# Kernel tuning notes

Measured on AMD Instinct MI355X. Metric: run time of the kernel, lower is better.

## Reference

```python
import jax, jax.numpy as jnp
import numpy as np

N = 200000      # nodes
E = 6400000     # edges (avg degree 32)
F_IN = 4        # node feature dim used by GraphConv
H = 184         # 4 * scale(46)
MD_H = 16       # min_distance MLP width
L1 = 188        # H + 4
A = 5           # action_space


def _uniform(k, shape, fan_in):
    b = 1.0 / np.sqrt(fan_in)
    return jax.random.uniform(k, shape, jnp.float32, -b, b)


def setup_inputs() -> dict:
    key = jax.random.key(0)
    ks = jax.random.split(key, 16)
    node_feat = jax.random.normal(ks[0], (N, 6), jnp.float32)
    edge_index = jax.random.randint(ks[1], (2, E), 0, N, dtype=jnp.int32)
    edge_weight = jax.random.uniform(ks[2], (E,), jnp.float32)
    center_idx = 0
    return {
        "node_feat": node_feat,
        "edge_index": edge_index,
        "edge_weight": edge_weight,
        "center_idx": center_idx,
        # GraphConv(4, 184): lin_rel (with bias) applied to aggregated msgs, lin_root (no bias) to x
        "W_rel": _uniform(ks[3], (F_IN, H), F_IN),
        "b_rel": _uniform(ks[4], (H,), F_IN),
        "W_root": _uniform(ks[5], (F_IN, H), F_IN),
        # linear2: 2 -> 16
        "W2": _uniform(ks[6], (2, MD_H), 2),
        "b2": _uniform(ks[7], (MD_H,), 2),
        # linear2_1: 16 -> 16
        "W21": _uniform(ks[8], (MD_H, MD_H), MD_H),
        "b21": _uniform(ks[9], (MD_H,), MD_H),
        # linear1: 200 -> 188
        "W1": _uniform(ks[10], (H + MD_H, L1), H + MD_H),
        "b1": _uniform(ks[11], (L1,), H + MD_H),
        # linear4: 188 -> 5
        "W4": _uniform(ks[12], (L1, A), L1),
        "b4": _uniform(ks[13], (A,), L1),
    }


def reference(node_feat, edge_index, edge_weight, center_idx,
              W_rel, b_rel, W_root, W2, b2, W21, b21, W1, b1, W4, b4):
    x = node_feat[:, :4]                                   # [N, 4]
    src, dst = edge_index[0], edge_index[1]
    # GraphConv message: e_ji * x_j, mean-aggregated at target nodes
    msg = x[src] * edge_weight[:, None]                    # [E, 4]
    agg = jax.ops.segment_sum(msg, dst, num_segments=N)    # [N, 4]
    deg = jax.ops.segment_sum(jnp.ones((E,), jnp.float32), dst, num_segments=N)
    mean = agg / jnp.maximum(deg, 1.0)[:, None]
    h = jax.nn.relu(mean @ W_rel + b_rel + x @ W_root)     # [N, 184]
    # global_max_pool with batch=None -> max over all nodes
    x1 = jnp.max(h, axis=0, keepdims=True)                 # [1, 184]
    x2 = h[center_idx:center_idx + 1]                      # [1, 184]
    g = x2 - x1
    md = node_feat[center_idx, 4:].reshape(1, 2)           # [1, 2]
    md = jax.nn.relu(md @ W2 + b2)
    md = jax.nn.relu(md @ W21 + b21)
    g = jnp.concatenate([g, md], axis=1)                   # [1, 200]
    g = jax.nn.relu(g @ W1 + b1)
    return g @ W4 + b4                                     # [1, 5]
```

## Files before the change

kernel.cpp:

```cpp
#include <hip/hip_runtime.h>

#define H 184
#define MDH 16
#define L1D 188
#define BBITS 9
#define BSZ 512
#define KMAX 512
#define CHUNKE 4096
#define SSUB 4
#define SREC_CAP 4416
#define HREC 2240
#define HRPT 5
#define NSPLIT 4

__global__ void zero_kernel(int* __restrict__ p, int n) {
    int i = blockIdx.x * blockDim.x + threadIdx.x;
    if (i < n) p[i] = 0;
}

__global__ __launch_bounds__(256) void pack_kernel(
        const float* __restrict__ nf, float4* __restrict__ x4,
        int* __restrict__ zp, int zn, int N) {
    __shared__ float s[256 * 6];
    int base = blockIdx.x * 256;
    int t = threadIdx.x;
    if (blockIdx.x == 0 && zp != nullptr)
        for (int i = t; i < zn; i += 256) zp[i] = 0;
    for (int i = t; i < 256 * 6; i += 256) {
        int gi = base * 6 + i;
        s[i] = (gi < N * 6) ? nf[gi] : 0.0f;
    }
    __syncthreads();
    int n = base + t;
    if (n < N)
        x4[n] = make_float4(s[t * 6], s[t * 6 + 1], s[t * 6 + 2], s[t * 6 + 3]);
}

__device__ __forceinline__ void scan512_w8(const int* __restrict__ cnt,
                                           int* __restrict__ sc,
                                           int* __restrict__ wtot, int t) {
    int wv = t >> 6, ln = t & 63;
    int x = cnt[t];
    #pragma unroll
    for (int d = 1; d < 64; d <<= 1) {
        int y = __shfl_up(x, d, 64);
        if (ln >= d) x += y;
    }
    if (ln == 63) wtot[wv] = x;
    __syncthreads();
    int woff = 0;
    #pragma unroll
    for (int wq = 0; wq < 7; ++wq) woff += (wq < wv) ? wtot[wq] : 0;
    sc[t] = woff + x;
    __syncthreads();
}

__global__ __launch_bounds__(512, 8) void partition_cs_kernel(
        const int* __restrict__ ei, const float* __restrict__ ew,
        int* __restrict__ cursor, uint2* __restrict__ region,
        const float* __restrict__ nf, float4* __restrict__ x4,
        int E, int K, int CAP, int N, int npack) {
    __shared__ uint2 srec[CHUNKE];
    __shared__ int cnt[KMAX];
    __shared__ int sc[KMAX];
    __shared__ int wbase[KMAX];
    __shared__ int wtot[8];
    int t = threadIdx.x;
    int c = blockIdx.x;

    if (c < npack) {
        float* sp = (float*)srec;
        int base = c * 256;
        for (int i = t; i < 256 * 6; i += 512) {
            int gi = base * 6 + i;
            sp[i] = (gi < N * 6) ? nf[gi] : 0.0f;
        }
        __syncthreads();
        if (t < 256) {
            int n = base + t;
            if (n < N)
                x4[n] = make_float4(sp[t * 6], sp[t * 6 + 1],
                                    sp[t * 6 + 2], sp[t * 6 + 3]);
        }
    }

    int e0 = c * CHUNKE;
    int e1 = min(E, e0 + CHUNKE);

    cnt[t] = 0;
    __syncthreads();

    unsigned meta[8];
    unsigned srcv[8];
    unsigned wv[8];
    #pragma unroll
    for (int j = 0; j < 2; ++j) {
        int e = e0 + t * 4 + j * 2048;
        int4 d4 = make_int4(0, 0, 0, 0);
        int4 s4 = make_int4(0, 0, 0, 0);
        float4 w4 = make_float4(0.f, 0.f, 0.f, 0.f);
        bool full = (e + 3 < e1);
        if (full) {
            d4 = *(const int4*)(ei + E + e);
            s4 = *(const int4*)(ei + e);
            w4 = *(const float4*)(ew + e);
        }
        #pragma unroll
        for (int q = 0; q < 4; ++q) {
            int idx = j * 4 + q;
            meta[idx] = 0xFFFFFFFFu;
            int eq = e + q;
            if (eq < e1) {
                int dst = full ? (q == 0 ? d4.x : q == 1 ? d4.y : q == 2 ? d4.z : d4.w)
                               : ei[E + eq];
                int src = full ? (q == 0 ? s4.x : q == 1 ? s4.y : q == 2 ? s4.z : s4.w)
                               : ei[eq];
                float w = full ? (q == 0 ? w4.x : q == 1 ? w4.y : q == 2 ? w4.z : w4.w)
                               : ew[eq];
                int k = ((unsigned)dst) >> BBITS;
                int r = atomicAdd(&cnt[k], 1);
                meta[idx] = ((unsigned)k << 21) | ((unsigned)r << 9)
                          | ((unsigned)dst & (BSZ - 1));
                srcv[idx] = (unsigned)src;
                wv[idx]   = __float_as_uint(w);
            }
        }
    }
    __syncthreads();

    scan512_w8(cnt, sc, wtot, t);

    {
        int ck = cnt[t];
        int pos = sc[t] - ck;
        int b = 0;
        if (t < K && ck > 0) {
            b = atomicAdd(&cursor[t], ck);
            if (b + ck > CAP) b = CAP - ck;
        }
        wbase[t] = b;
        cnt[t] = pos;
    }
    __syncthreads();

    #pragma unroll
    for (int j = 0; j < 8; ++j) {
        if (meta[j] != 0xFFFFFFFFu) {
            int k  = meta[j] >> 21;
            int r  = (meta[j] >> 9) & 0xFFF;
            int dl = meta[j] & (BSZ - 1);
            int slot = cnt[k] + r;
            srec[slot] = make_uint2(((unsigned)dl << 18) | srcv[j], wv[j]);
        }
    }
    __syncthreads();

    {
        int pos = cnt[t];
        int ck = sc[t] - pos;
        if (t < K && ck > 0) {
            uint2* dstp = region + (size_t)t * CAP + wbase[t];
            for (int i = 0; i < ck; ++i)
                dstp[i] = srec[pos + i];
        }
    }
}

__global__ __launch_bounds__(512, 8) void bucket_sort_accum_kernel(
        const float4* __restrict__ x4, const uint2* __restrict__ region,
        const int* __restrict__ cursor, float* __restrict__ partials, int CAP) {
    __shared__ float4 sxw[HREC];
    __shared__ int cnt[BSZ], sc[BSZ];
    __shared__ int wtot[8];
    int k = blockIdx.x / SSUB;
    int s = blockIdx.x % SSUB;
    int t = threadIdx.x;

    int len = cursor[k];
    if (len > CAP) len = CAP;
    const uint2* base = region + (size_t)k * CAP;
    int i0 = (int)(((long long)len * s) / SSUB);
    int i1 = (int)(((long long)len * (s + 1)) / SSUB);
    int span = i1 - i0;

    float4 acc = make_float4(0.f, 0.f, 0.f, 0.f);
    int degc = 0;

    #pragma unroll
    for (int half = 0; half < 2; ++half) {
        int h0 = i0 + (span * half) / 2;
        int h1 = i0 + (span * (half + 1)) / 2;
        cnt[t] = 0;
        __syncthreads();

        float4 xw[HRPT];
        unsigned rb[HRPT];
        #pragma unroll
        for (int j = 0; j < HRPT; ++j) {
            int i = h0 + t + j * 512;
            rb[j] = 0xFFFFFFFFu;
            if (i < h1) {
                uint2 r = base[i];
                int bin = r.x >> 18;
                float4 xv = x4[r.x & 0x3FFFFu];
                float w = __uint_as_float(r.y);
                xw[j] = make_float4(xv.x * w, xv.y * w, xv.z * w, xv.w * w);
                int rk = atomicAdd(&cnt[bin], 1);
                rb[j] = ((unsigned)bin << 13) | (unsigned)rk;
            }
        }
        __syncthreads();

        scan512_w8(cnt, sc, wtot, t);

        #pragma unroll
        for (int j = 0; j < HRPT; ++j) {
            if (rb[j] != 0xFFFFFFFFu) {
                int bin = rb[j] >> 13;
                int rk  = rb[j] & 0x1FFF;
                sxw[sc[bin] - cnt[bin] + rk] = xw[j];
            }
        }
        __syncthreads();

        int c = cnt[t], st = sc[t] - c;
        for (int i = 0; i < c; ++i) {
            float4 v = sxw[st + i];
            acc.x += v.x; acc.y += v.y; acc.z += v.z; acc.w += v.w;
        }
        degc += c;
        __syncthreads();
    }

    float* pp = partials + (size_t)blockIdx.x * (BSZ * 5);
    pp[0 * BSZ + t] = acc.x;
    pp[1 * BSZ + t] = acc.y;
    pp[2 * BSZ + t] = acc.z;
    pp[3 * BSZ + t] = acc.w;
    pp[4 * BSZ + t] = (float)degc;
}

__global__ __launch_bounds__(256) void edge_atomic_kernel(
        const float* __restrict__ nf, const int* __restrict__ ei,
        const float* __restrict__ ew, float* __restrict__ agg,
        float* __restrict__ deg, int E) {
    int e = blockIdx.x * blockDim.x + threadIdx.x;
    if (e >= E) return;
    int src = ei[e];
    int dst = ei[E + e];
    float w = ew[e];
    const float2* xr = (const float2*)(nf + (size_t)src * 6);
    float2 x01 = xr[0];
    float2 x23 = xr[1];
    float* a = agg + (size_t)dst * 4;
    atomicAdd(a + 0, x01.x * w);
    atomicAdd(a + 1, x01.y * w);
    atomicAdd(a + 2, x23.x * w);
    atomicAdd(a + 3, x23.y * w);
    atomicAdd(deg + dst, 1.0f);
}

__global__ __launch_bounds__(256) void node_bucket_kernel(
        const float4* __restrict__ x4,
        const float* __restrict__ partials,
        const float* __restrict__ W_rel, const float* __restrict__ b_rel,
        const float* __restrict__ W_root,
        const int*   __restrict__ centerp,
        unsigned int* __restrict__ xmax_bits,
        float* __restrict__ h0,
        int N) {
    __shared__ float4 xm[BSZ / NSPLIT];
    __shared__ float4 xt[BSZ / NSPLIT];
    const int NB = BSZ / NSPLIT;
    int k = blockIdx.x / NSPLIT;
    int q = blockIdx.x % NSPLIT;
    int t = threadIdx.x;
    int center = *centerp;
    int base_d = q * NB;
    int nmax = min(BSZ, N - (k << BBITS));
    int cnt_local = min(NB, nmax - base_d);
    if (cnt_local <= 0) return;
    const float* bp = partials + (size_t)k * SSUB * (BSZ * 5);

    if (t < NB) {
        int d = base_d + t;
        float a0 = 0.f, a1 = 0.f, a2 = 0.f, a3 = 0.f, dg = 0.f;
        #pragma unroll
        for (int s = 0; s < SSUB; ++s) {
            const float* p = bp + (size_t)s * (BSZ * 5);
            a0 += p[0 * BSZ + d];
            a1 += p[1 * BSZ + d];
            a2 += p[2 * BSZ + d];
            a3 += p[3 * BSZ + d];
            dg += p[4 * BSZ + d];
        }
        float inv = 1.0f / fmaxf(dg, 1.0f);
        xm[t] = make_float4(a0 * inv, a1 * inv, a2 * inv, a3 * inv);
    } else {
        int i = t - NB;
        int n = (k << BBITS) + base_d + i;
        xt[i] = (n < N) ? x4[n] : make_float4(0.f, 0.f, 0.f, 0.f);
    }
    __syncthreads();

    int j = t;
    if (j >= H) return;

    float wr0 = W_rel[0 * H + j], wr1 = W_rel[1 * H + j];
    float wr2 = W_rel[2 * H + j], wr3 = W_rel[3 * H + j];
    float wo0 = W_root[0 * H + j], wo1 = W_root[1 * H + j];
    float wo2 = W_root[2 * H + j], wo3 = W_root[3 * H + j];
    float b = b_rel[j];

    int cd = ((center >> BBITS) == k) ? (center & (BSZ - 1)) - base_d : -1;
    float mx = 0.0f;
    for (int i = 0; i < cnt_local; ++i) {
        float4 m = xm[i];
        float4 x = xt[i];
        float v = b
                + m.x * wr0 + m.y * wr1 + m.z * wr2 + m.w * wr3
                + x.x * wo0 + x.y * wo1 + x.z * wo2 + x.w * wo3;
        v = fmaxf(v, 0.0f);
        mx = fmaxf(mx, v);
        if (i == cd) h0[j] = v;
    }
    atomicMax(xmax_bits + j, __float_as_uint(mx));
}

__global__ __launch_bounds__(192) void node_kernel(
        const float4* __restrict__ x4,
        const float* __restrict__ agg,
        const float* __restrict__ deg,
        const float* __restrict__ W_rel, const float* __restrict__ b_rel,
        const float* __restrict__ W_root,
        const int*   __restrict__ centerp,
        unsigned int* __restrict__ xmax_bits,
        float* __restrict__ h0,
        int N, int nodes_per_block) {
    int j = threadIdx.x;
    if (j >= H) return;
    int center = *centerp;
    int n0 = blockIdx.x * nodes_per_block;
    int n1 = n0 + nodes_per_block;
    if (n1 > N) n1 = N;

    float wr0 = W_rel[0 * H + j], wr1 = W_rel[1 * H + j];
    float wr2 = W_rel[2 * H + j], wr3 = W_rel[3 * H + j];
    float wo0 = W_root[0 * H + j], wo1 = W_root[1 * H + j];
    float wo2 = W_root[2 * H + j], wo3 = W_root[3 * H + j];
    float b = b_rel[j];

    float mx = 0.0f;
    for (int n = n0; n < n1; ++n) {
        float4 a = ((const float4*)agg)[n];
        float inv = 1.0f / fmaxf(deg[n], 1.0f);
        float4 x = x4[n];
        float v = b
                + (a.x * inv) * wr0 + (a.y * inv) * wr1
                + (a.z * inv) * wr2 + (a.w * inv) * wr3
                + x.x * wo0 + x.y * wo1 + x.z * wo2 + x.w * wo3;
        v = fmaxf(v, 0.0f);
        mx = fmaxf(mx, v);
        if (n == center) h0[j] = v;
    }
    atomicMax(xmax_bits + j, __float_as_uint(mx));
}

__global__ __launch_bounds__(768) void final_kernel(
        const float* __restrict__ nf,
        const int*   __restrict__ centerp,
        const unsigned int* __restrict__ xmax_bits,
        const float* __restrict__ h0,
        const float* __restrict__ W2,  const float* __restrict__ b2,
        const float* __restrict__ W21, const float* __restrict__ b21,
        const float* __restrict__ W1,  const float* __restrict__ b1,
        const float* __restrict__ W4,  const float* __restrict__ b4,
        float* __restrict__ out) {
    __shared__ float gin[H + MDH];
    __shared__ float md0[MDH];
    __shared__ float part[4][L1D];
    __shared__ float g1[L1D];
    int t = threadIdx.x;
    int center = *centerp;

    if (t < H) gin[t] = h0[t] - __uint_as_float(xmax_bits[t]);
    if (t < MDH) {
        float m0 = nf[(size_t)center * 6 + 4];
        float m1 = nf[(size_t)center * 6 + 5];
        md0[t] = fmaxf(m0 * W2[t] + m1 * W2[MDH + t] + b2[t], 0.0f);
    }
    __syncthreads();
    if (t < MDH) {
        float s = b21[t];
        for (int k = 0; k < MDH; ++k) s += md0[k] * W21[k * MDH + t];
        gin[H + t] = fmaxf(s, 0.0f);
    }
    __syncthreads();

    {
        int kc = t / 192;
        int j  = t - kc * 192;
        if (j < L1D) {
            float s = 0.0f;
            int k0 = kc * 50, k1 = k0 + 50;
            #pragma unroll 5
            for (int k = k0; k < k1; ++k) s += gin[k] * W1[k * L1D + j];
            part[kc][j] = s;
        }
    }
    __syncthreads();
    if (t < L1D)
        g1[t] = fmaxf(part[0][t] + part[1][t] + part[2][t] + part[3][t] + b1[t],
                      0.0f);
    __syncthreads();

    int w = t >> 6, ln = t & 63;
    if (w < 5) {
        float s = 0.0f;
        for (int k = ln; k < L1D; k += 64) s += g1[k] * W4[k * 5 + w];
        #pragma unroll
        for (int d = 32; d > 0; d >>= 1) s += __shfl_down(s, d, 64);
        if (ln == 0) out[w] = s + b4[w];
    }
}

extern "C" void kernel_launch(void* const* d_in, const int* in_sizes, int n_in,
                              void* d_out, int out_size, void* d_ws, size_t ws_size,
                              hipStream_t stream) {
    const float* nf      = (const float*)d_in[0];
    const int*   ei      = (const int*)  d_in[1];
    const float* ew      = (const float*)d_in[2];
    const int*   centerp = (const int*)  d_in[3];
    const float* W_rel   = (const float*)d_in[4];
    const float* b_rel   = (const float*)d_in[5];
    const float* W_root  = (const float*)d_in[6];
    const float* W2      = (const float*)d_in[7];
    const float* b2      = (const float*)d_in[8];
    const float* W21     = (const float*)d_in[9];
    const float* b21     = (const float*)d_in[10];
    const float* W1      = (const float*)d_in[11];
    const float* b1      = (const float*)d_in[12];
    const float* W4      = (const float*)d_in[13];
    const float* b4      = (const float*)d_in[14];
    float* out = (float*)d_out;

    const int N = in_sizes[0] / 6;
    const int E = in_sizes[1] / 2;
    const int K = (N + BSZ - 1) >> BBITS;
    const int nchunks = (E + CHUNKE - 1) / CHUNKE;
    const int npack = (N + 255) / 256;
    int cap = E / K + E / K / 16 + 256;
    cap = (cap + 63) & ~63;

    int*          cursor   = (int*)d_ws;
    unsigned int* xmax     = (unsigned int*)(cursor + 512);
    float*        h0       = (float*)(xmax + H);
    float*        agg      = h0 + H;
    float*        deg      = agg + (size_t)N * 4;
    float4*       x4       = (float4*)(deg + N);
    float*        partials = (float*)(x4 + N);
    uint2*        region   = (uint2*)(partials + (size_t)K * SSUB * (BSZ * 5));

    size_t need = (size_t)((char*)(region + (size_t)K * cap) - (char*)d_ws);
    bool fast = (ws_size >= need) && (K <= KMAX) && (N <= (1 << 18))
             && ((E & 3) == 0)
             && ((cap + SSUB - 1) / SSUB <= SREC_CAP)
             && (((cap + SSUB - 1) / SSUB + 1) / 2 <= HREC)
             && (npack <= nchunks);

    if (fast) {
        hipMemsetAsync(cursor, 0, (size_t)(512 + H) * sizeof(int), stream);
        partition_cs_kernel<<<nchunks, 512, 0, stream>>>(ei, ew, cursor, region,
                                                         nf, x4, E, K, cap,
                                                         N, npack);
        bucket_sort_accum_kernel<<<K * SSUB, 512, 0, stream>>>(x4, region, cursor,
                                                               partials, cap);
        node_bucket_kernel<<<K * NSPLIT, 256, 0, stream>>>(x4, partials,
                                                           W_rel, b_rel, W_root,
                                                           centerp, xmax, h0, N);
    } else {
        const int blocks = 2048;
        const int npb = (N + blocks - 1) / blocks;
        zero_kernel<<<(N * 5 + 255) / 256, 256, 0, stream>>>((int*)agg, N * 5);
        zero_kernel<<<1, 256, 0, stream>>>(cursor, 512 + H);
        pack_kernel<<<(N + 255) / 256, 256, 0, stream>>>(nf, x4, nullptr, 0, N);
        edge_atomic_kernel<<<(E + 255) / 256, 256, 0, stream>>>(nf, ei, ew, agg, deg, E);
        node_kernel<<<blocks, 192, 0, stream>>>(x4, agg, deg,
                                                W_rel, b_rel, W_root,
                                                centerp, xmax, h0, N, npb);
    }

    final_kernel<<<1, 768, 0, stream>>>(nf, centerp, xmax, h0,
                                        W2, b2, W21, b21, W1, b1, W4, b4, out);
}
```

Before: 270.1 us.

## Defer src/weight loads to scatter phase and split partition launch in two

The partition kernel now loads only destination indices before the histogram and scan, and reads source indices and weights later, just before writing the shared-memory records. This cuts the per-thread register arrays held across the barriers, which may raise occupancy, but it puts the src and weight loads after the synchronisations, where they are harder to overlap. The partition grid is also split into two launches with a block offset, which adds launch overhead and a serialisation point between the halves.

```diff
diff --git a/kernel.cpp b/kernel.cpp
--- a/kernel.cpp
+++ b/kernel.cpp
@@ -59,14 +59,14 @@
         const int* __restrict__ ei, const float* __restrict__ ew,
         int* __restrict__ cursor, uint2* __restrict__ region,
         const float* __restrict__ nf, float4* __restrict__ x4,
-        int E, int K, int CAP, int N, int npack) {
+        int E, int K, int CAP, int N, int npack, int c0) {
     __shared__ uint2 srec[CHUNKE];
     __shared__ int cnt[KMAX];
     __shared__ int sc[KMAX];
     __shared__ int wbase[KMAX];
     __shared__ int wtot[8];
     int t = threadIdx.x;
-    int c = blockIdx.x;
+    int c = blockIdx.x + c0;
 
     if (c < npack) {
         float* sp = (float*)srec;
@@ -91,20 +91,12 @@
     __syncthreads();
 
     unsigned meta[8];
-    unsigned srcv[8];
-    unsigned wv[8];
     #pragma unroll
     for (int j = 0; j < 2; ++j) {
         int e = e0 + t * 4 + j * 2048;
         int4 d4 = make_int4(0, 0, 0, 0);
-        int4 s4 = make_int4(0, 0, 0, 0);
-        float4 w4 = make_float4(0.f, 0.f, 0.f, 0.f);
         bool full = (e + 3 < e1);
-        if (full) {
-            d4 = *(const int4*)(ei + E + e);
-            s4 = *(const int4*)(ei + e);
-            w4 = *(const float4*)(ew + e);
-        }
+        if (full) d4 = *(const int4*)(ei + E + e);
         #pragma unroll
         for (int q = 0; q < 4; ++q) {
             int idx = j * 4 + q;
@@ -113,16 +105,10 @@
             if (eq < e1) {
                 int dst = full ? (q == 0 ? d4.x : q == 1 ? d4.y : q == 2 ? d4.z : d4.w)
                                : ei[E + eq];
-                int src = full ? (q == 0 ? s4.x : q == 1 ? s4.y : q == 2 ? s4.z : s4.w)
-                               : ei[eq];
-                float w = full ? (q == 0 ? w4.x : q == 1 ? w4.y : q == 2 ? w4.z : w4.w)
-                               : ew[eq];
                 int k = ((unsigned)dst) >> BBITS;
                 int r = atomicAdd(&cnt[k], 1);
                 meta[idx] = ((unsigned)k << 21) | ((unsigned)r << 9)
                           | ((unsigned)dst & (BSZ - 1));
-                srcv[idx] = (unsigned)src;
-                wv[idx]   = __float_as_uint(w);
             }
         }
     }
@@ -144,13 +130,30 @@
     __syncthreads();
 
     #pragma unroll
-    for (int j = 0; j < 8; ++j) {
-        if (meta[j] != 0xFFFFFFFFu) {
-            int k  = meta[j] >> 21;
-            int r  = (meta[j] >> 9) & 0xFFF;
-            int dl = meta[j] & (BSZ - 1);
-            int slot = cnt[k] + r;
-            srec[slot] = make_uint2(((unsigned)dl << 18) | srcv[j], wv[j]);
+    for (int j = 0; j < 2; ++j) {
+        int e = e0 + t * 4 + j * 2048;
+        int4 s4 = make_int4(0, 0, 0, 0);
+        float4 w4 = make_float4(0.f, 0.f, 0.f, 0.f);
+        bool full = (e + 3 < e1);
+        if (full) {
+            s4 = *(const int4*)(ei + e);
+            w4 = *(const float4*)(ew + e);
+        }
+        #pragma unroll
+        for (int q = 0; q < 4; ++q) {
+            int idx = j * 4 + q;
+            int eq = e + q;
+            if (meta[idx] != 0xFFFFFFFFu) {
+                int src = full ? (q == 0 ? s4.x : q == 1 ? s4.y : q == 2 ? s4.z : s4.w)
+                               : ei[eq];
+                float w = full ? (q == 0 ? w4.x : q == 1 ? w4.y : q == 2 ? w4.z : w4.w)
+                               : ew[eq];
+                int k  = meta[idx] >> 21;
+                int r  = (meta[idx] >> 9) & 0xFFF;
+                int dl = meta[idx] & (BSZ - 1);
+                srec[cnt[k] + r] = make_uint2(((unsigned)dl << 18) | (unsigned)src,
+                                              __float_as_uint(w));
+            }
         }
     }
     __syncthreads();
@@ -462,17 +465,22 @@
     uint2*        region   = (uint2*)(partials + (size_t)K * SSUB * (BSZ * 5));
 
     size_t need = (size_t)((char*)(region + (size_t)K * cap) - (char*)d_ws);
+    const int nb1 = (nchunks + 1) / 2;
+    const int nb2 = nchunks - nb1;
     bool fast = (ws_size >= need) && (K <= KMAX) && (N <= (1 << 18))
              && ((E & 3) == 0)
              && ((cap + SSUB - 1) / SSUB <= SREC_CAP)
              && (((cap + SSUB - 1) / SSUB + 1) / 2 <= HREC)
-             && (npack <= nchunks);
+             && (npack <= nb1) && (nb2 > 0);
 
     if (fast) {
         hipMemsetAsync(cursor, 0, (size_t)(512 + H) * sizeof(int), stream);
-        partition_cs_kernel<<<nchunks, 512, 0, stream>>>(ei, ew, cursor, region,
-                                                         nf, x4, E, K, cap,
-                                                         N, npack);
+        partition_cs_kernel<<<nb1, 512, 0, stream>>>(ei, ew, cursor, region,
+                                                     nf, x4, E, K, cap,
+                                                     N, npack, 0);
+        partition_cs_kernel<<<nb2, 512, 0, stream>>>(ei, ew, cursor, region,
+                                                     nf, x4, E, K, cap,
+                                                     N, npack, nb1);
         bucket_sort_accum_kernel<<<K * SSUB, 512, 0, stream>>>(x4, region, cursor,
                                                                partials, cap);
         node_bucket_kernel<<<K * NSPLIT, 256, 0, stream>>>(x4, partials,
```

After: 292.7 us. 8.4% more time.

## Fuse bucket accumulation with node transform into a single per-bucket kernel

Applied to the files above, without the earlier changes.

Merges the bucketed edge accumulation and the per-node GraphConv, ReLU and max kernel into one kernel with one block per destination bucket. Each block now walks its whole bucket in shared-memory-sized chunks instead of splitting it across four sub-blocks. This removes the partials buffer round-trip through global memory and one kernel launch. The cost is four times fewer blocks during the gather-heavy accumulation phase, so there is less parallelism to hide memory latency. Capacity guards tied to the old split are dropped.

```diff
diff --git a/kernel.cpp b/kernel.cpp
--- a/kernel.cpp
+++ b/kernel.cpp
@@ -8,10 +8,8 @@
 #define KMAX 512
 #define CHUNKE 4096
 #define SSUB 4
-#define SREC_CAP 4416
 #define HREC 2240
 #define HRPT 5
-#define NSPLIT 4
 
 __global__ void zero_kernel(int* __restrict__ p, int n) {
     int i = blockIdx.x * blockDim.x + threadIdx.x;
@@ -149,8 +147,7 @@
             int k  = meta[j] >> 21;
             int r  = (meta[j] >> 9) & 0xFFF;
             int dl = meta[j] & (BSZ - 1);
-            int slot = cnt[k] + r;
-            srec[slot] = make_uint2(((unsigned)dl << 18) | srcv[j], wv[j]);
+            srec[cnt[k] + r] = make_uint2(((unsigned)dl << 18) | srcv[j], wv[j]);
         }
     }
     __syncthreads();
@@ -166,30 +163,30 @@
     }
 }
 
-__global__ __launch_bounds__(512, 8) void bucket_sort_accum_kernel(
+__global__ __launch_bounds__(512, 8) void accum_node_kernel(
         const float4* __restrict__ x4, const uint2* __restrict__ region,
-        const int* __restrict__ cursor, float* __restrict__ partials, int CAP) {
+        const int* __restrict__ cursor,
+        const float* __restrict__ W_rel, const float* __restrict__ b_rel,
+        const float* __restrict__ W_root,
+        const int*   __restrict__ centerp,
+        unsigned int* __restrict__ xmax_bits,
+        float* __restrict__ h0,
+        int CAP, int N) {
     __shared__ float4 sxw[HREC];
     __shared__ int cnt[BSZ], sc[BSZ];
     __shared__ int wtot[8];
-    int k = blockIdx.x / SSUB;
-    int s = blockIdx.x % SSUB;
+    int k = blockIdx.x;
     int t = threadIdx.x;
 
     int len = cursor[k];
     if (len > CAP) len = CAP;
     const uint2* base = region + (size_t)k * CAP;
-    int i0 = (int)(((long long)len * s) / SSUB);
-    int i1 = (int)(((long long)len * (s + 1)) / SSUB);
-    int span = i1 - i0;
 
     float4 acc = make_float4(0.f, 0.f, 0.f, 0.f);
     int degc = 0;
 
-    #pragma unroll
-    for (int half = 0; half < 2; ++half) {
-        int h0 = i0 + (span * half) / 2;
-        int h1 = i0 + (span * (half + 1)) / 2;
+    for (int c0 = 0; c0 < len; c0 += HREC) {
+        int c1 = min(len, c0 + HREC);
         cnt[t] = 0;
         __syncthreads();
 
@@ -197,9 +194,9 @@
         unsigned rb[HRPT];
         #pragma unroll
         for (int j = 0; j < HRPT; ++j) {
-            int i = h0 + t + j * 512;
+            int i = c0 + t + j * 512;
             rb[j] = 0xFFFFFFFFu;
-            if (i < h1) {
+            if (i < c1) {
                 uint2 r = base[i];
                 int bin = r.x >> 18;
                 float4 xv = x4[r.x & 0x3FFFFu];
@@ -232,12 +229,44 @@
         __syncthreads();
     }
 
-    float* pp = partials + (size_t)blockIdx.x * (BSZ * 5);
-    pp[0 * BSZ + t] = acc.x;
-    pp[1 * BSZ + t] = acc.y;
-    pp[2 * BSZ + t] = acc.z;
-    pp[3 * BSZ + t] = acc.w;
-    pp[4 * BSZ + t] = (float)degc;
+    float4* xm = sxw;
+    float4* xt = sxw + BSZ;
+    int n = (k << BBITS) + t;
+    float inv = 1.0f / fmaxf((float)degc, 1.0f);
+    xm[t] = make_float4(acc.x * inv, acc.y * inv, acc.z * inv, acc.w * inv);
+    xt[t] = (n < N) ? x4[n] : make_float4(0.f, 0.f, 0.f, 0.f);
+    __syncthreads();
+
+    int nmax = min(BSZ, N - (k << BBITS));
+    int center = *centerp;
+    int cloc = ((center >> BBITS) == k) ? (center & (BSZ - 1)) : -1;
+    float* pm = (float*)cnt;
+    int halfg = (t >= 256) ? 1 : 0;
+    int j = t - halfg * 256;
+    if (j < H) {
+        float wr0 = W_rel[0 * H + j], wr1 = W_rel[1 * H + j];
+        float wr2 = W_rel[2 * H + j], wr3 = W_rel[3 * H + j];
+        float wo0 = W_root[0 * H + j], wo1 = W_root[1 * H + j];
+        float wo2 = W_root[2 * H + j], wo3 = W_root[3 * H + j];
+        float b = b_rel[j];
+        int ibeg = halfg * 256;
+        int iend = min(ibeg + 256, nmax);
+        float mx = 0.0f;
+        for (int i = ibeg; i < iend; ++i) {
+            float4 m = xm[i];
+            float4 x = xt[i];
+            float v = b
+                    + m.x * wr0 + m.y * wr1 + m.z * wr2 + m.w * wr3
+                    + x.x * wo0 + x.y * wo1 + x.z * wo2 + x.w * wo3;
+            v = fmaxf(v, 0.0f);
+            mx = fmaxf(mx, v);
+            if (i == cloc) h0[j] = v;
+        }
+        pm[halfg * H + j] = mx;
+    }
+    __syncthreads();
+    if (t < H)
+        atomicMax(xmax_bits + t, __float_as_uint(fmaxf(pm[t], pm[H + t])));
 }
 
 __global__ __launch_bounds__(256) void edge_atomic_kernel(
@@ -258,73 +287,6 @@
     atomicAdd(a + 2, x23.x * w);
     atomicAdd(a + 3, x23.y * w);
     atomicAdd(deg + dst, 1.0f);
-}
-
-__global__ __launch_bounds__(256) void node_bucket_kernel(
-        const float4* __restrict__ x4,
-        const float* __restrict__ partials,
-        const float* __restrict__ W_rel, const float* __restrict__ b_rel,
-        const float* __restrict__ W_root,
-        const int*   __restrict__ centerp,
-        unsigned int* __restrict__ xmax_bits,
-        float* __restrict__ h0,
-        int N) {
-    __shared__ float4 xm[BSZ / NSPLIT];
-    __shared__ float4 xt[BSZ / NSPLIT];
-    const int NB = BSZ / NSPLIT;
-    int k = blockIdx.x / NSPLIT;
-    int q = blockIdx.x % NSPLIT;
-    int t = threadIdx.x;
-    int center = *centerp;
-    int base_d = q * NB;
-    int nmax = min(BSZ, N - (k << BBITS));
-    int cnt_local = min(NB, nmax - base_d);
-    if (cnt_local <= 0) return;
-    const float* bp = partials + (size_t)k * SSUB * (BSZ * 5);
-
-    if (t < NB) {
-        int d = base_d + t;
-        float a0 = 0.f, a1 = 0.f, a2 = 0.f, a3 = 0.f, dg = 0.f;
-        #pragma unroll
-        for (int s = 0; s < SSUB; ++s) {
-            const float* p = bp + (size_t)s * (BSZ * 5);
-            a0 += p[0 * BSZ + d];
-            a1 += p[1 * BSZ + d];
-            a2 += p[2 * BSZ + d];
-            a3 += p[3 * BSZ + d];
-            dg += p[4 * BSZ + d];
-        }
-        float inv = 1.0f / fmaxf(dg, 1.0f);
-        xm[t] = make_float4(a0 * inv, a1 * inv, a2 * inv, a3 * inv);
-    } else {
-        int i = t - NB;
-        int n = (k << BBITS) + base_d + i;
-        xt[i] = (n < N) ? x4[n] : make_float4(0.f, 0.f, 0.f, 0.f);
-    }
-    __syncthreads();
-
-    int j = t;
-    if (j >= H) return;
-
-    float wr0 = W_rel[0 * H + j], wr1 = W_rel[1 * H + j];
-    float wr2 = W_rel[2 * H + j], wr3 = W_rel[3 * H + j];
-    float wo0 = W_root[0 * H + j], wo1 = W_root[1 * H + j];
-    float wo2 = W_root[2 * H + j], wo3 = W_root[3 * H + j];
-    float b = b_rel[j];
-
-    int cd = ((center >> BBITS) == k) ? (center & (BSZ - 1)) - base_d : -1;
-    float mx = 0.0f;
-    for (int i = 0; i < cnt_local; ++i) {
-        float4 m = xm[i];
-        float4 x = xt[i];
-        float v = b
-                + m.x * wr0 + m.y * wr1 + m.z * wr2 + m.w * wr3
-                + x.x * wo0 + x.y * wo1 + x.z * wo2 + x.w * wo3;
-        v = fmaxf(v, 0.0f);
-        mx = fmaxf(mx, v);
-        if (i == cd) h0[j] = v;
-    }
-    atomicMax(xmax_bits + j, __float_as_uint(mx));
 }
 
 __global__ __launch_bounds__(192) void node_kernel(
@@ -464,8 +426,6 @@
     size_t need = (size_t)((char*)(region + (size_t)K * cap) - (char*)d_ws);
     bool fast = (ws_size >= need) && (K <= KMAX) && (N <= (1 << 18))
              && ((E & 3) == 0)
-             && ((cap + SSUB - 1) / SSUB <= SREC_CAP)
-             && (((cap + SSUB - 1) / SSUB + 1) / 2 <= HREC)
              && (npack <= nchunks);
 
     if (fast) {
@@ -473,11 +433,9 @@
         partition_cs_kernel<<<nchunks, 512, 0, stream>>>(ei, ew, cursor, region,
                                                          nf, x4, E, K, cap,
                                                          N, npack);
-        bucket_sort_accum_kernel<<<K * SSUB, 512, 0, stream>>>(x4, region, cursor,
-                                                               partials, cap);
-        node_bucket_kernel<<<K * NSPLIT, 256, 0, stream>>>(x4, partials,
-                                                           W_rel, b_rel, W_root,
-                                                           centerp, xmax, h0, N);
+        accum_node_kernel<<<K, 512, 0, stream>>>(x4, region, cursor,
+                                                 W_rel, b_rel, W_root,
+                                                 centerp, xmax, h0, cap, N);
     } else {
         const int blocks = 2048;
         const int npb = (N + blocks - 1) / blocks;
```

Result: slower. 276.0 us (+2.2%).

## Fuse bucket accumulation, node transform and final MLP into one cooperative kernel

Applied to the files above, without the earlier changes.

Replaces the bucket_sort_accum, node_bucket and final kernels with a single cooperative-launch kernel that processes the same work items in grid-stride loops, separated by grid-wide syncs. The goal is to remove two kernel launches and the gaps between them. The cost is two grid.sync barriers, a persistent grid of 768–1024 blocks that may be less balanced than the original launch shapes, and dependence on cooperative launch succeeding. If that launch fails, the code falls back to the old three-kernel path.

```diff
diff --git a/kernel.cpp b/kernel.cpp
--- a/kernel.cpp
+++ b/kernel.cpp
@@ -1,4 +1,7 @@
 #include <hip/hip_runtime.h>
+#include <hip/hip_cooperative_groups.h>
+
+namespace cg = cooperative_groups;
 
 #define H 184
 #define MDH 16
@@ -8,7 +11,6 @@
 #define KMAX 512
 #define CHUNKE 4096
 #define SSUB 4
-#define SREC_CAP 4416
 #define HREC 2240
 #define HRPT 5
 #define NSPLIT 4
@@ -149,8 +151,7 @@
             int k  = meta[j] >> 21;
             int r  = (meta[j] >> 9) & 0xFFF;
             int dl = meta[j] & (BSZ - 1);
-            int slot = cnt[k] + r;
-            srec[slot] = make_uint2(((unsigned)dl << 18) | srcv[j], wv[j]);
+            srec[cnt[k] + r] = make_uint2(((unsigned)dl << 18) | srcv[j], wv[j]);
         }
     }
     __syncthreads();
@@ -162,6 +163,201 @@
             uint2* dstp = region + (size_t)t * CAP + wbase[t];
             for (int i = 0; i < ck; ++i)
                 dstp[i] = srec[pos + i];
+        }
+    }
+}
+
+__global__ __launch_bounds__(512, 8) void fused_tail_kernel(
+        const float4* __restrict__ x4, const uint2* __restrict__ region,
+        const int* __restrict__ cursor, float* __restrict__ partials,
+        const float* __restrict__ W_rel, const float* __restrict__ b_rel,
+        const float* __restrict__ W_root,
+        const int*   __restrict__ centerp,
+        unsigned int* __restrict__ xmax_bits, float* __restrict__ h0,
+        const float* __restrict__ nf,
+        const float* __restrict__ W2,  const float* __restrict__ b2,
+        const float* __restrict__ W21, const float* __restrict__ b21,
+        const float* __restrict__ W1,  const float* __restrict__ b1,
+        const float* __restrict__ W4,  const float* __restrict__ b4,
+        float* __restrict__ out,
+        int CAP, int N, int K, int nitems) {
+    __shared__ float4 sxw[HREC];
+    __shared__ int cnt[BSZ], sc[BSZ];
+    __shared__ int wtot[8];
+    cg::grid_group grid = cg::this_grid();
+    int t = threadIdx.x;
+
+    for (int wi = blockIdx.x; wi < nitems; wi += gridDim.x) {
+        int k = wi / SSUB, s = wi - (wi / SSUB) * SSUB;
+        int len = cursor[k];
+        if (len > CAP) len = CAP;
+        const uint2* rbase = region + (size_t)k * CAP;
+        int i0 = (int)(((long long)len * s) / SSUB);
+        int i1 = (int)(((long long)len * (s + 1)) / SSUB);
+        int span = i1 - i0;
+
+        float4 acc = make_float4(0.f, 0.f, 0.f, 0.f);
+        int degc = 0;
+
+        #pragma unroll
+        for (int half = 0; half < 2; ++half) {
+            int hb = i0 + (span * half) / 2;
+            int he = i0 + (span * (half + 1)) / 2;
+            cnt[t] = 0;
+            __syncthreads();
+
+            float4 xw[HRPT];
+            unsigned rb[HRPT];
+            #pragma unroll
+            for (int j = 0; j < HRPT; ++j) {
+                int i = hb + t + j * 512;
+                rb[j] = 0xFFFFFFFFu;
+                if (i < he) {
+                    uint2 r = rbase[i];
+                    int bin = r.x >> 18;
+                    float4 xv = x4[r.x & 0x3FFFFu];
+                    float w = __uint_as_float(r.y);
+                    xw[j] = make_float4(xv.x * w, xv.y * w, xv.z * w, xv.w * w);
+                    int rk = atomicAdd(&cnt[bin], 1);
+                    rb[j] = ((unsigned)bin << 13) | (unsigned)rk;
+                }
+            }
+            __syncthreads();
+
+            scan512_w8(cnt, sc, wtot, t);
+
+            #pragma unroll
+            for (int j = 0; j < HRPT; ++j) {
+                if (rb[j] != 0xFFFFFFFFu) {
+                    int bin = rb[j] >> 13;
+                    int rk  = rb[j] & 0x1FFF;
+                    sxw[sc[bin] - cnt[bin] + rk] = xw[j];
+                }
+            }
+            __syncthreads();
+
+            int c = cnt[t], st = sc[t] - c;
+            for (int i = 0; i < c; ++i) {
+                float4 v = sxw[st + i];
+                acc.x += v.x; acc.y += v.y; acc.z += v.z; acc.w += v.w;
+            }
+            degc += c;
+            __syncthreads();
+        }
+
+        float* pp = partials + (size_t)wi * (BSZ * 5);
+        pp[0 * BSZ + t] = acc.x;
+        pp[1 * BSZ + t] = acc.y;
+        pp[2 * BSZ + t] = acc.z;
+        pp[3 * BSZ + t] = acc.w;
+        pp[4 * BSZ + t] = (float)degc;
+    }
+
+    grid.sync();
+
+    int center = *centerp;
+    for (int wi = blockIdx.x; wi < K * NSPLIT; wi += gridDim.x) {
+        int k = wi >> 2, q = wi & 3;
+        int base_d = q * 128;
+        float4* xm = sxw;
+        float4* xt = sxw + 128;
+        if (t < 128) {
+            int d = base_d + t;
+            float a0 = 0.f, a1 = 0.f, a2 = 0.f, a3 = 0.f, dg = 0.f;
+            const float* bp = partials + (size_t)k * SSUB * (BSZ * 5);
+            #pragma unroll
+            for (int s = 0; s < SSUB; ++s) {
+                const float* p = bp + (size_t)s * (BSZ * 5);
+                a0 += p[0 * BSZ + d];
+                a1 += p[1 * BSZ + d];
+                a2 += p[2 * BSZ + d];
+                a3 += p[3 * BSZ + d];
+                dg += p[4 * BSZ + d];
+            }
+            float inv = 1.0f / fmaxf(dg, 1.0f);
+            xm[t] = make_float4(a0 * inv, a1 * inv, a2 * inv, a3 * inv);
+        } else if (t < 256) {
+            int i = t - 128;
+            int n = (k << BBITS) + base_d + i;
+            xt[i] = (n < N) ? x4[n] : make_float4(0.f, 0.f, 0.f, 0.f);
+        }
+        __syncthreads();
+
+        int nmax = min(BSZ, N - (k << BBITS));
+        int cnt_local = min(128, nmax - base_d);
+        float* pm = (float*)cnt;
+        int halfg = (t >= 256) ? 1 : 0;
+        int j = t - halfg * 256;
+        if (cnt_local > 0 && j < H) {
+            float wr0 = W_rel[0 * H + j], wr1 = W_rel[1 * H + j];
+            float wr2 = W_rel[2 * H + j], wr3 = W_rel[3 * H + j];
+            float wo0 = W_root[0 * H + j], wo1 = W_root[1 * H + j];
+            float wo2 = W_root[2 * H + j], wo3 = W_root[3 * H + j];
+            float b = b_rel[j];
+            int cloc = ((center >> BBITS) == k) ? (center & (BSZ - 1)) - base_d : -1;
+            int ib = halfg * 64;
+            int ie = min(ib + 64, cnt_local);
+            float mx = 0.0f;
+            for (int i = ib; i < ie; ++i) {
+                float4 m = xm[i];
+                float4 x = xt[i];
+                float v = b
+                        + m.x * wr0 + m.y * wr1 + m.z * wr2 + m.w * wr3
+                        + x.x * wo0 + x.y * wo1 + x.z * wo2 + x.w * wo3;
+                v = fmaxf(v, 0.0f);
+                mx = fmaxf(mx, v);
+                if (i == cloc) h0[j] = v;
+            }
+            pm[halfg * H + j] = mx;
+        }
+        __syncthreads();
+        if (cnt_local > 0 && t < H)
+            atomicMax(xmax_bits + t, __float_as_uint(fmaxf(pm[t], pm[H + t])));
+        __syncthreads();
+    }
+
+    grid.sync();
+
+    if (blockIdx.x == 0) {
+        float* gin = (float*)sxw;
+        float* md0 = gin + 256;
+        float* pt  = md0 + 32;
+        float* g1  = pt + 2 * L1D;
+        if (t < H) gin[t] = h0[t] - __uint_as_float(xmax_bits[t]);
+        if (t < MDH) {
+            float m0 = nf[(size_t)center * 6 + 4];
+            float m1 = nf[(size_t)center * 6 + 5];
+            md0[t] = fmaxf(m0 * W2[t] + m1 * W2[MDH + t] + b2[t], 0.0f);
+        }
+        __syncthreads();
+        if (t < MDH) {
+            float s2 = b21[t];
+            for (int kk = 0; kk < MDH; ++kk) s2 += md0[kk] * W21[kk * MDH + t];
+            gin[H + t] = fmaxf(s2, 0.0f);
+        }
+        __syncthreads();
+        {
+            int kc = t >> 8;
+            int j  = t & 255;
+            if (j < L1D) {
+                float s2 = 0.0f;
+                int k0 = kc * 100, k1 = k0 + 100;
+                #pragma unroll 4
+                for (int kk = k0; kk < k1; ++kk) s2 += gin[kk] * W1[kk * L1D + j];
+                pt[kc * L1D + j] = s2;
+            }
+        }
+        __syncthreads();
+        if (t < L1D)
+            g1[t] = fmaxf(pt[t] + pt[L1D + t] + b1[t], 0.0f);
+        __syncthreads();
+        int w = t >> 6, ln = t & 63;
+        if (w < 5) {
+            float s2 = 0.0f;
+            for (int kk = ln; kk < L1D; kk += 64) s2 += g1[kk] * W4[kk * 5 + w];
+            #pragma unroll
+            for (int d = 32; d > 0; d >>= 1) s2 += __shfl_down(s2, d, 64);
+            if (ln == 0) out[w] = s2 + b4[w];
         }
     }
 }
@@ -188,8 +384,8 @@
 
     #pragma unroll
     for (int half = 0; half < 2; ++half) {
-        int h0 = i0 + (span * half) / 2;
-        int h1 = i0 + (span * (half + 1)) / 2;
+        int h0i = i0 + (span * half) / 2;
+        int h1i = i0 + (span * (half + 1)) / 2;
         cnt[t] = 0;
         __syncthreads();
 
@@ -197,9 +393,9 @@
         unsigned rb[HRPT];
         #pragma unroll
         for (int j = 0; j < HRPT; ++j) {
-            int i = h0 + t + j * 512;
+            int i = h0i + t + j * 512;
             rb[j] = 0xFFFFFFFFu;
-            if (i < h1) {
+            if (i < h1i) {
                 uint2 r = base[i];
                 int bin = r.x >> 18;
                 float4 xv = x4[r.x & 0x3FFFFu];
@@ -210,9 +406,7 @@
             }
         }
         __syncthreads();
-
         scan512_w8(cnt, sc, wtot, t);
-
         #pragma unroll
         for (int j = 0; j < HRPT; ++j) {
             if (rb[j] != 0xFFFFFFFFu) {
@@ -222,7 +416,6 @@
             }
         }
         __syncthreads();
-
         int c = cnt[t], st = sc[t] - c;
         for (int i = 0; i < c; ++i) {
             float4 v = sxw[st + i];
@@ -238,26 +431,6 @@
     pp[2 * BSZ + t] = acc.z;
     pp[3 * BSZ + t] = acc.w;
     pp[4 * BSZ + t] = (float)degc;
-}
-
-__global__ __launch_bounds__(256) void edge_atomic_kernel(
-        const float* __restrict__ nf, const int* __restrict__ ei,
-        const float* __restrict__ ew, float* __restrict__ agg,
-        float* __restrict__ deg, int E) {
-    int e = blockIdx.x * blockDim.x + threadIdx.x;
-    if (e >= E) return;
-    int src = ei[e];
-    int dst = ei[E + e];
-    float w = ew[e];
-    const float2* xr = (const float2*)(nf + (size_t)src * 6);
-    float2 x01 = xr[0];
-    float2 x23 = xr[1];
-    float* a = agg + (size_t)dst * 4;
-    atomicAdd(a + 0, x01.x * w);
-    atomicAdd(a + 1, x01.y * w);
-    atomicAdd(a + 2, x23.x * w);
-    atomicAdd(a + 3, x23.y * w);
-    atomicAdd(deg + dst, 1.0f);
 }
 
 __global__ __launch_bounds__(256) void node_bucket_kernel(
@@ -327,6 +500,26 @@
     atomicMax(xmax_bits + j, __float_as_uint(mx));
 }
 
+__global__ __launch_bounds__(256) void edge_atomic_kernel(
+        const float* __restrict__ nf, const int* __restrict__ ei,
+        const float* __restrict__ ew, float* __restrict__ agg,
+        float* __restrict__ deg, int E) {
+    int e = blockIdx.x * blockDim.x + threadIdx.x;
+    if (e >= E) return;
+    int src = ei[e];
+    int dst = ei[E + e];
+    float w = ew[e];
+    const float2* xr = (const float2*)(nf + (size_t)src * 6);
+    float2 x01 = xr[0];
+    float2 x23 = xr[1];
+    float* a = agg + (size_t)dst * 4;
+    atomicAdd(a + 0, x01.x * w);
+    atomicAdd(a + 1, x01.y * w);
+    atomicAdd(a + 2, x23.x * w);
+    atomicAdd(a + 3, x23.y * w);
+    atomicAdd(deg + dst, 1.0f);
+}
+
 __global__ __launch_bounds__(192) void node_kernel(
         const float4* __restrict__ x4,
         const float* __restrict__ agg,
@@ -396,7 +589,6 @@
         gin[H + t] = fmaxf(s, 0.0f);
     }
     __syncthreads();
-
     {
         int kc = t / 192;
         int j  = t - kc * 192;
@@ -413,7 +605,6 @@
         g1[t] = fmaxf(part[0][t] + part[1][t] + part[2][t] + part[3][t] + b1[t],
                       0.0f);
     __syncthreads();
-
     int w = t >> 6, ln = t & 63;
     if (w < 5) {
         float s = 0.0f;
@@ -464,20 +655,41 @@
     size_t need = (size_t)((char*)(region + (size_t)K * cap) - (char*)d_ws);
     bool fast = (ws_size >= need) && (K <= KMAX) && (N <= (1 << 18))
              && ((E & 3) == 0)
-             && ((cap + SSUB - 1) / SSUB <= SREC_CAP)
-             && (((cap + SSUB - 1) / SSUB + 1) / 2 <= HREC)
+             && ((((cap + SSUB - 1) / SSUB) + 1) / 2 <= HREC)
              && (npack <= nchunks);
 
+    bool need_final = true;
     if (fast) {
         hipMemsetAsync(cursor, 0, (size_t)(512 + H) * sizeof(int), stream);
         partition_cs_kernel<<<nchunks, 512, 0, stream>>>(ei, ew, cursor, region,
                                                          nf, x4, E, K, cap,
                                                          N, npack);
-        bucket_sort_accum_kernel<<<K * SSUB, 512, 0, stream>>>(x4, region, cursor,
-                                                               partials, cap);
-        node_bucket_kernel<<<K * NSPLIT, 256, 0, stream>>>(x4, partials,
-                                                           W_rel, b_rel, W_root,
-                                                           centerp, xmax, h0, N);
+        int nitems = K * SSUB;
+        const float4* x4c = x4;
+        const uint2* regc = region;
+        const int* curc = cursor;
+        void* cargs[] = {
+            (void*)&x4c, (void*)&regc, (void*)&curc, (void*)&partials,
+            (void*)&W_rel, (void*)&b_rel, (void*)&W_root,
+            (void*)&centerp, (void*)&xmax, (void*)&h0, (void*)&nf,
+            (void*)&W2, (void*)&b2, (void*)&W21, (void*)&b21,
+            (void*)&W1, (void*)&b1, (void*)&W4, (void*)&b4,
+            (void*)&out, (void*)&cap, (void*)&N, (void*)&K, (void*)&nitems
+        };
+        hipError_t ce = hipErrorUnknown;
+        for (int g = 1024; g >= 768; g -= 256) {
+            ce = hipLaunchCooperativeKernel((const void*)fused_tail_kernel,
+                                            dim3(g), dim3(512), cargs, 0, stream);
+            if (ce == hipSuccess) break;
+        }
+        if (ce == hipSuccess) {
+            need_final = false;
+        } else {
+            bucket_sort_accum_kernel<<<K * SSUB, 512, 0, stream>>>(
+                x4, region, cursor, partials, cap);
+            node_bucket_kernel<<<K * NSPLIT, 256, 0, stream>>>(
+                x4, partials, W_rel, b_rel, W_root, centerp, xmax, h0, N);
+        }
     } else {
         const int blocks = 2048;
         const int npb = (N + blocks - 1) / blocks;
@@ -490,6 +702,7 @@
                                                 centerp, xmax, h0, N, npb);
     }
 
-    final_kernel<<<1, 768, 0, stream>>>(nf, centerp, xmax, h0,
-                                        W2, b2, W21, b21, W1, b1, W4, b4, out);
-}
+    if (need_final)
+        final_kernel<<<1, 768, 0, stream>>>(nf, centerp, xmax, h0,
+                                            W2, b2, W21, b21, W1, b1, W4, b4, out);
+}
```

Result: slower. 551.5 us (+104.2%).
